# Performance work log

Measured on AMD Instinct MI355X. Metric: run time of the kernel, lower is better.

## Reference

```python
import jax, jax.numpy as jnp
import numpy as np
import math

# Model hyperparameters (SchNet defaults)
H = 128        # hidden_channels
F = 128        # num_filters
G = 50         # num_gaussians
CUT = 6.0      # cutoff (Angstrom)
L_INT = 3      # num_interactions
# Graph scale
N_MOL = 512    # molecules
APM = 32       # atoms per molecule
N = N_MOL * APM
BOX = 10.0     # side of cubic box per molecule


def _ssp(x):
    # ShiftedSoftplus
    return jax.nn.softplus(x) - math.log(2.0)


def setup_inputs() -> dict:
    rng = np.random.default_rng(0)
    pos = rng.uniform(0.0, BOX, (N_MOL, APM, 3)).astype(np.float32)
    # radius graph within each molecule (faithful to radius_graph_custom,
    # precomputed here because edge count is data-dependent)
    srcs, dsts = [], []
    for m in range(N_MOL):
        p = pos[m]
        dm = np.linalg.norm(p[:, None, :] - p[None, :, :], axis=-1)
        mask = dm <= CUT
        np.fill_diagonal(mask, False)
        s, t = np.nonzero(mask)
        srcs.append(s + m * APM)
        dsts.append(t + m * APM)
    edge_index = np.stack([np.concatenate(srcs), np.concatenate(dsts)]).astype(np.int32)
    pos = pos.reshape(N, 3)
    batch = np.repeat(np.arange(N_MOL, dtype=np.int32), APM)
    z = rng.integers(1, 100, N).astype(np.int32)

    key = jax.random.key(0)
    ks = jax.random.split(key, 16)
    s = 0.1
    nrm = lambda k, shp: (jax.random.normal(k, shp, dtype=jnp.float32) * s)
    return {
        "z": jnp.asarray(z),
        "pos": jnp.asarray(pos),
        "batch": jnp.asarray(batch),
        "edge_index": jnp.asarray(edge_index),
        "emb": nrm(ks[0], (100, H)),
        "mlp_w1": nrm(ks[1], (L_INT, G, F)),
        "mlp_b1": jnp.zeros((L_INT, F), jnp.float32),
        "mlp_w2": nrm(ks[2], (L_INT, F, F)),
        "mlp_b2": jnp.zeros((L_INT, F), jnp.float32),
        "cf1_w": nrm(ks[3], (L_INT, H, F)),
        "cf2_w": nrm(ks[4], (L_INT, F, H)),
        "cf2_b": jnp.zeros((L_INT, H), jnp.float32),
        "lin_w": nrm(ks[5], (L_INT, H, H)),
        "lin_b": jnp.zeros((L_INT, H), jnp.float32),
        "out1_w": nrm(ks[6], (H, H // 2)),
        "out1_b": jnp.zeros((H // 2,), jnp.float32),
        "out2_w": nrm(ks[7], (H // 2, 1)),
        "out2_b": jnp.zeros((1,), jnp.float32),
    }


def reference(z, pos, batch, edge_index, emb,
              mlp_w1, mlp_b1, mlp_w2, mlp_b2,
              cf1_w, cf2_w, cf2_b, lin_w, lin_b,
              out1_w, out1_b, out2_w, out2_b):
    src, dst = edge_index[0], edge_index[1]
    # edge_weight = euclidean distance (== cdist[src, dst])
    d = jnp.sqrt(jnp.sum((pos[src] - pos[dst]) ** 2, axis=-1))  # [E]
    # GaussianSmearing
    offs = jnp.linspace(0.0, CUT, G)
    coeff = -0.5 / (CUT / (G - 1)) ** 2
    edge_attr = jnp.exp(coeff * (d[:, None] - offs[None, :]) ** 2)  # [E, G]
    # cosine cutoff
    Ccut = 0.5 * (jnp.cos(d * math.pi / CUT) + 1.0)  # [E]

    h = emb[z]  # [N, H]
    for l in range(L_INT):
        # edge filter MLP with cutoff
        W = _ssp(edge_attr @ mlp_w1[l] + mlp_b1[l]) @ mlp_w2[l] + mlp_b2[l]  # [E, F]
        W = W * Ccut[:, None]
        # CFConv: lin1 -> gather x_j -> multiply -> scatter-add to dst -> lin2
        msg = (h @ cf1_w[l])[src] * W                                # [E, F]
        agg = jax.ops.segment_sum(msg, dst, num_segments=N)          # [N, F]
        v = agg @ cf2_w[l] + cf2_b[l]                                # [N, H]
        v = _ssp(v)
        v = v @ lin_w[l] + lin_b[l]
        h = h + v  # residual

    h = _ssp(h @ out1_w + out1_b)
    h = h @ out2_w + out2_b                                          # [N, 1]
    out = jax.ops.segment_sum(h, batch, num_segments=N_MOL)          # [N_MOL, 1]
    return out
```

## Files before the change

### kernel.cpp

```cpp
#include <hip/hip_runtime.h>
#include <hip/hip_bf16.h>
#include <hip/hip_fp16.h>
#include <math.h>

#define NATOMS 16384
#define NMOL   512
#define APM    32
#define GDIM   50
#define KTAB   4096

#define STRH 132
#define STRA 136

typedef __attribute__((ext_vector_type(8))) short   short8;
typedef __attribute__((ext_vector_type(4))) float   floatx4;

__device__ __forceinline__ float ssp(float x) {
    float e = __expf(-fabsf(x));
    return fmaxf(x, 0.0f) + __logf(1.0f + e) - 0.69314718055994531f;
}

__device__ __forceinline__ unsigned short f2bf(float x) {
    union { float f; unsigned int u; } v; v.f = x;
    unsigned int lsb = (v.u >> 16) & 1u;
    v.u += 0x7fffu + lsb;
    return (unsigned short)(v.u >> 16);
}

__device__ __forceinline__ unsigned short f2h(float x) {
    __half h = __float2half(x);
    unsigned short u;
    __builtin_memcpy(&u, &h, 2);
    return u;
}

__device__ __forceinline__ unsigned int pk2bf(float a, float b) {
    __hip_bfloat162 h = __float22bfloat162_rn(make_float2(a, b));
    unsigned int u;
    __builtin_memcpy(&u, &h, 4);
    return u;
}

#define KW1 72
#define KW2 136
#define NTILE (KTAB / 64)

__global__ __launch_bounds__(256) void mega_setup_kernel(
    const float* __restrict__ pos,
    unsigned* __restrict__ koG,
    const float* __restrict__ cf1, const float* __restrict__ cf2,
    const float* __restrict__ lin, const float* __restrict__ out1,
    unsigned short* __restrict__ Wtall,
    const float* __restrict__ w1_, const float* __restrict__ b1_,
    const float* __restrict__ w2_, const float* __restrict__ b2_,
    unsigned short* __restrict__ Tt)
{
    const int WB = (9 * 16384 + 64 * 128 + 255) / 256;
    const int b = blockIdx.x;
    const int tid = threadIdx.x;

    __shared__ float sp[96];

    if (b < NMOL) {
        if (tid < 96) sp[tid] = pos[b * 96 + tid];
        if (b < 3 && tid < 128)
            Tt[(size_t)b * (KTAB + 1) * 128 + (size_t)KTAB * 128 + tid] = 0;
        __syncthreads();
        #pragma unroll
        for (int c4 = 0; c4 < 4; c4++) {
            int c = c4 * 256 + tid;
            int i = c >> 5, j = c & 31;
            float dx = sp[3 * i]     - sp[3 * j];
            float dy = sp[3 * i + 1] - sp[3 * j + 1];
            float dz = sp[3 * i + 2] - sp[3 * j + 2];
            float d  = sqrtf(dx * dx + dy * dy + dz * dz);
            unsigned off = (unsigned)(KTAB << 8);
            if (i != j && d <= 6.0f) {
                float u = d * (float)(KTAB - 1) / 6.0f;
                int k = min((int)(u + 0.5f), KTAB - 1);
                off = (unsigned)(k << 8);
            }
            koG[((size_t)b << 10) + c] = off;
        }
        return;
    }
    if (b < NMOL + WB) {
        int idx = (b - NMOL) * 256 + tid;
        if (idx < 9 * 16384) {
            int wi = idx >> 14, rem = idx & 16383;
            int n = rem >> 7, k = rem & 127;
            int l = wi / 3, which = wi % 3;
            const float* src = (which == 0) ? cf1 : (which == 1) ? cf2 : lin;
            Wtall[idx] = f2bf(src[(size_t)l * 16384 + k * 128 + n]);
        } else if (idx < 9 * 16384 + 64 * 128) {
            int q = idx - 9 * 16384;
            int n = q >> 7, k = q & 127;
            Wtall[idx] = f2bf(out1[k * 64 + n]);
        }
        return;
    }

    __shared__ unsigned short s_bufA[128 * KW2];
    __shared__ unsigned short s_bufB[128 * KW1];

    const int tt = b - NMOL - WB;
    const int l  = tt / NTILE;
    const int bx = tt % NTILE;
    const float* w1 = w1_ + (size_t)l * GDIM * 128;
    const float* b1 = b1_ + (size_t)l * 128;
    const float* w2 = w2_ + (size_t)l * 128 * 128;
    const float* b2 = b2_ + (size_t)l * 128;
    unsigned short* Tg = Tt + (size_t)l * (KTAB + 1) * 128;

    unsigned short* s_w1T = s_bufB;
    unsigned short* s_w2T = s_bufA;
    unsigned short* s_t   = s_bufB;

    for (int i = tid; i < GDIM * 128; i += 256) {
        int g = i >> 7, f = i & 127;
        s_w1T[f * KW1 + g] = f2bf(w1[i]);
    }
    for (int i = tid; i < (64 - GDIM) * 128; i += 256) {
        int g = GDIM + (i >> 7), f = i & 127;
        s_w1T[f * KW1 + g] = 0;
    }
    for (int i = tid; i < 128 * 128; i += 256) {
        int k = i >> 7, n = i & 127;
        s_w2T[n * KW2 + k] = f2bf(w2[i]);
    }

    const int lane = tid & 63;
    const int w    = tid >> 6;
    const int l15  = lane & 15;
    const int quad = lane >> 4;

    float b1v[8], b2v[8];
    #pragma unroll
    for (int nt = 0; nt < 8; nt++) {
        b1v[nt] = b1[nt * 16 + l15];
        b2v[nt] = b2[nt * 16 + l15];
    }
    __syncthreads();

    const float hstep = 6.0f / (float)(KTAB - 1);
    const float step  = 6.0f / 49.0f;
    const float coeff = -0.5f / (step * step);
    const float pioc  = 3.14159265358979323846f / 6.0f;
    const int k0 = bx * 64;
    const float dm = (float)(k0 + w * 16 + l15) * hstep;

    floatx4 acc1[8];
    #pragma unroll
    for (int nt = 0; nt < 8; nt++) acc1[nt] = (floatx4){0.f, 0.f, 0.f, 0.f};
    #pragma unroll
    for (int ks = 0; ks < 2; ks++) {
        unsigned int ap[4];
        #pragma unroll
        for (int jj = 0; jj < 4; jj++) {
            int g0 = ks * 32 + quad * 8 + 2 * jj;
            float d0 = dm - (float)g0 * step;
            float d1 = dm - (float)(g0 + 1) * step;
            float v0 = (g0 < GDIM)     ? __expf(coeff * d0 * d0) : 0.0f;
            float v1 = (g0 + 1 < GDIM) ? __expf(coeff * d1 * d1) : 0.0f;
            ap[jj] = pk2bf(v0, v1);
        }
        short8 af;
        __builtin_memcpy(&af, ap, 16);
        #pragma unroll
        for (int nt = 0; nt < 8; nt++) {
            short8 bfg = *(const short8*)&s_w1T[(nt * 16 + l15) * KW1 + ks * 32 + quad * 8];
            acc1[nt] = __builtin_amdgcn_mfma_f32_16x16x32_bf16(af, bfg, acc1[nt], 0, 0, 0);
        }
    }
    __syncthreads();

    #pragma unroll
    for (int nt = 0; nt < 8; nt++) {
        #pragma unroll
        for (int r = 0; r < 4; r++) {
            int row = w * 16 + quad * 4 + r;
            s_t[row * KW2 + nt * 16 + l15] = f2bf(ssp(acc1[nt][r] + b1v[nt]));
        }
    }

    floatx4 acc2[8];
    #pragma unroll
    for (int nt = 0; nt < 8; nt++) acc2[nt] = (floatx4){0.f, 0.f, 0.f, 0.f};
    #pragma unroll
    for (int ks = 0; ks < 4; ks++) {
        short8 af = *(const short8*)&s_t[(w * 16 + l15) * KW2 + ks * 32 + quad * 8];
        #pragma unroll
        for (int nt = 0; nt < 8; nt++) {
            short8 bfg = *(const short8*)&s_w2T[(nt * 16 + l15) * KW2 + ks * 32 + quad * 8];
            acc2[nt] = __builtin_amdgcn_mfma_f32_16x16x32_bf16(af, bfg, acc2[nt], 0, 0, 0);
        }
    }

    #pragma unroll
    for (int nt = 0; nt < 8; nt++) {
        #pragma unroll
        for (int r = 0; r < 4; r++) {
            int row = w * 16 + quad * 4 + r;
            float d = (float)(k0 + row) * hstep;
            float cut = 0.5f * (__cosf(d * pioc) + 1.0f);
            Tg[(size_t)(k0 + row) * 128 + nt * 16 + l15] = f2h((acc2[nt][r] + b2v[nt]) * cut);
        }
    }
}

__global__ __launch_bounds__(512, 4) void fused_schnet_kernel(
    const int* __restrict__ z, const float* __restrict__ emb,
    const unsigned* __restrict__ koG,
    const unsigned short* __restrict__ Tt,
    const unsigned short* __restrict__ Wtall,
    const float* __restrict__ cf2_b, const float* __restrict__ lin_b,
    const float* __restrict__ out1_b, const float* __restrict__ out2_w,
    const float* __restrict__ out2_b,
    float* __restrict__ out)
{
    __shared__ float s_h[32 * STRH];
    __shared__ float s_hx[32 * 128];
    __shared__ unsigned short s_agg[32 * STRA];
    __shared__ unsigned int s_ko[32 * 32];
    __shared__ float s_red;
    unsigned short* s_t = (unsigned short*)s_hx;

    const int tid  = threadIdx.x;
    const int lane = tid & 63;
    const int w    = tid >> 6;
    const int l15  = lane & 15;
    const int quad = lane >> 4;
    const int r16  = (w & 1) * 16;
    const int c32  = (w >> 1) * 32;
    const int B0   = blockIdx.x * 32;

    const unsigned lOff = (unsigned)(lane << 2);

    for (int i = tid; i < 32 * 128; i += 512) {
        int row = i >> 7, col = i & 127;
        s_h[row * STRH + col] = emb[(size_t)z[B0 + row] * 128 + col];
    }
    for (int i = tid; i < 1024; i += 512)
        s_ko[i] = koG[((size_t)blockIdx.x << 10) + i];
    if (tid == 0) s_red = 0.0f;

    __syncthreads();

    const unsigned short* WtO = Wtall + 9 * 16384;

#define KO_RFL(KO, SC)                                                        \
    _Pragma("unroll")                                                         \
    for (int i = 0; i < 4; i++) {                                             \
        uint4 ka = *(const uint4*)&s_ko[(((w << 2) + i) << 5) + ((SC) << 3)]; \
        uint4 kb = *(const uint4*)&s_ko[(((w << 2) + i) << 5) + ((SC) << 3) + 4]; \
        KO[i][0] = __builtin_amdgcn_readfirstlane(ka.x);                      \
        KO[i][1] = __builtin_amdgcn_readfirstlane(ka.y);                      \
        KO[i][2] = __builtin_amdgcn_readfirstlane(ka.z);                      \
        KO[i][3] = __builtin_amdgcn_readfirstlane(ka.w);                      \
        KO[i][4] = __builtin_amdgcn_readfirstlane(kb.x);                      \
        KO[i][5] = __builtin_amdgcn_readfirstlane(kb.y);                      \
        KO[i][6] = __builtin_amdgcn_readfirstlane(kb.z);                      \
        KO[i][7] = __builtin_amdgcn_readfirstlane(kb.w);                      \
    }
#define TP_LOAD(TP, KO)                                                       \
    _Pragma("unroll")                                                         \
    for (int i = 0; i < 4; i++) {                                             \
        _Pragma("unroll")                                                     \
        for (int j = 0; j < 8; j++)                                           \
            TP[i][j] = *(const unsigned*)(TlB + KO[i][j] + lOff);             \
    }
#define FMA_CHUNK(TP, SC)                                                     \
    _Pragma("unroll")                                                         \
    for (int j = 0; j < 8; j++) {                                             \
        float2 hv = *(const float2*)&s_hx[((((SC) << 3) + j) << 7) + (lane << 1)]; \
        _Pragma("unroll")                                                     \
        for (int i = 0; i < 4; i++) {                                         \
            unsigned t = TP[i][j];                                            \
            asm("v_fma_mix_f32 %0, %1, %2, %0 op_sel:[0,0,0] op_sel_hi:[1,0,0]" \
                : "+v"(a0[i]) : "v"(t), "v"(hv.x));                           \
            asm("v_fma_mix_f32 %0, %1, %2, %0 op_sel:[1,0,0] op_sel_hi:[1,0,0]" \
                : "+v"(a1[i]) : "v"(t), "v"(hv.y));                           \
        }                                                                     \
    }

    for (int l = 0; l < 3; l++) {
        const unsigned short* W1 = Wtall + (size_t)(l * 3 + 0) * 16384;
        const unsigned short* W2 = Wtall + (size_t)(l * 3 + 1) * 16384;
        const unsigned short* W3 = Wtall + (size_t)(l * 3 + 2) * 16384;
        const char* TlB = (const char*)(Tt + (size_t)l * (KTAB + 1) * 128);

        floatx4 acc[2];
        #pragma unroll
        for (int nt = 0; nt < 2; nt++) acc[nt] = (floatx4){0.f, 0.f, 0.f, 0.f};
        #pragma unroll
        for (int ks = 0; ks < 4; ks++) {
            const float* hp = &s_h[(r16 + l15) * STRH + ks * 32 + quad * 8];
            float4 xa = *(const float4*)hp;
            float4 xb = *(const float4*)(hp + 4);
            unsigned int ap[4];
            ap[0] = pk2bf(xa.x, xa.y); ap[1] = pk2bf(xa.z, xa.w);
            ap[2] = pk2bf(xb.x, xb.y); ap[3] = pk2bf(xb.z, xb.w);
            short8 af;
            __builtin_memcpy(&af, ap, 16);
            #pragma unroll
            for (int nt = 0; nt < 2; nt++) {
                short8 bfg = *(const short8*)&W1[(size_t)(c32 + nt * 16 + l15) * 128 + ks * 32 + quad * 8];
                acc[nt] = __builtin_amdgcn_mfma_f32_16x16x32_bf16(af, bfg, acc[nt], 0, 0, 0);
            }
        }
        #pragma unroll
        for (int nt = 0; nt < 2; nt++) {
            #pragma unroll
            for (int r = 0; r < 4; r++)
                s_hx[(r16 + quad * 4 + r) * 128 + c32 + nt * 16 + l15] = acc[nt][r];
        }

        __syncthreads();

        {
            float a0[4], a1[4];
            #pragma unroll
            for (int i = 0; i < 4; i++) { a0[i] = 0.0f; a1[i] = 0.0f; }

            unsigned koA[4][8], koB[4][8], tpA[4][8], tpB[4][8];
            KO_RFL(koA, 0)
            TP_LOAD(tpA, koA)

            KO_RFL(koB, 1)
            TP_LOAD(tpB, koB)
            FMA_CHUNK(tpA, 0)

            KO_RFL(koA, 2)
            TP_LOAD(tpA, koA)
            FMA_CHUNK(tpB, 1)

            KO_RFL(koB, 3)
            TP_LOAD(tpB, koB)
            FMA_CHUNK(tpA, 2)

            FMA_CHUNK(tpB, 3)

            #pragma unroll
            for (int i = 0; i < 4; i++)
                *(unsigned*)&s_agg[((w << 2) + i) * STRA + (lane << 1)] = pk2bf(a0[i], a1[i]);
        }

        __syncthreads();

        float bva[2], bvb[2];
        #pragma unroll
        for (int nt = 0; nt < 2; nt++) {
            bva[nt] = cf2_b[l * 128 + c32 + nt * 16 + l15];
            bvb[nt] = lin_b[l * 128 + c32 + nt * 16 + l15];
        }
        #pragma unroll
        for (int nt = 0; nt < 2; nt++) acc[nt] = (floatx4){0.f, 0.f, 0.f, 0.f};
        #pragma unroll
        for (int ks = 0; ks < 4; ks++) {
            short8 af = *(const short8*)&s_agg[(r16 + l15) * STRA + ks * 32 + quad * 8];
            #pragma unroll
            for (int nt = 0; nt < 2; nt++) {
                short8 bfg = *(const short8*)&W2[(size_t)(c32 + nt * 16 + l15) * 128 + ks * 32 + quad * 8];
                acc[nt] = __builtin_amdgcn_mfma_f32_16x16x32_bf16(af, bfg, acc[nt], 0, 0, 0);
            }
        }
        #pragma unroll
        for (int nt = 0; nt < 2; nt++) {
            #pragma unroll
            for (int r = 0; r < 4; r++) {
                int row = r16 + quad * 4 + r;
                s_t[row * STRA + c32 + nt * 16 + l15] = f2bf(ssp(acc[nt][r] + bva[nt]));
            }
        }

        __syncthreads();

        #pragma unroll
        for (int nt = 0; nt < 2; nt++) acc[nt] = (floatx4){0.f, 0.f, 0.f, 0.f};
        #pragma unroll
        for (int ks = 0; ks < 4; ks++) {
            short8 af = *(const short8*)&s_t[(r16 + l15) * STRA + ks * 32 + quad * 8];
            #pragma unroll
            for (int nt = 0; nt < 2; nt++) {
                short8 bfg = *(const short8*)&W3[(size_t)(c32 + nt * 16 + l15) * 128 + ks * 32 + quad * 8];
                acc[nt] = __builtin_amdgcn_mfma_f32_16x16x32_bf16(af, bfg, acc[nt], 0, 0, 0);
            }
        }
        #pragma unroll
        for (int nt = 0; nt < 2; nt++) {
            #pragma unroll
            for (int r = 0; r < 4; r++) {
                int row = r16 + quad * 4 + r;
                s_h[row * STRH + c32 + nt * 16 + l15] += acc[nt][r] + bvb[nt];
            }
        }
        __syncthreads();
    }

    const int c16 = (w >> 1) * 16;
    floatx4 ha = (floatx4){0.f, 0.f, 0.f, 0.f};
    #pragma unroll
    for (int ks = 0; ks < 4; ks++) {
        const float* hp = &s_h[(r16 + l15) * STRH + ks * 32 + quad * 8];
        float4 xa = *(const float4*)hp;
        float4 xb = *(const float4*)(hp + 4);
        unsigned int ap[4];
        ap[0] = pk2bf(xa.x, xa.y); ap[1] = pk2bf(xa.z, xa.w);
        ap[2] = pk2bf(xb.x, xb.y); ap[3] = pk2bf(xb.z, xb.w);
        short8 af;
        __builtin_memcpy(&af, ap, 16);
        short8 bfg = *(const short8*)&WtO[(size_t)(c16 + l15) * 128 + ks * 32 + quad * 8];
        ha = __builtin_amdgcn_mfma_f32_16x16x32_bf16(af, bfg, ha, 0, 0, 0);
    }
    float part = 0.0f;
    {
        float b1o = out1_b[c16 + l15];
        float o2  = out2_w[c16 + l15];
        #pragma unroll
        for (int r = 0; r < 4; r++)
            part += ssp(ha[r] + b1o) * o2;
    }
    #pragma unroll
    for (int off = 32; off > 0; off >>= 1) part += __shfl_down(part, off);
    if (lane == 0) atomicAdd(&s_red, part);
    __syncthreads();
    if (tid == 0) out[blockIdx.x] = s_red + 32.0f * out2_b[0];

#undef KO_RFL
#undef TP_LOAD
#undef FMA_CHUNK
}

extern "C" void kernel_launch(void* const* d_in, const int* in_sizes, int n_in,
                              void* d_out, int out_size, void* d_ws, size_t ws_size,
                              hipStream_t stream)
{
    const int*   z      = (const int*)d_in[0];
    const float* pos    = (const float*)d_in[1];
    const float* emb    = (const float*)d_in[4];
    const float* mlp_w1 = (const float*)d_in[5];
    const float* mlp_b1 = (const float*)d_in[6];
    const float* mlp_w2 = (const float*)d_in[7];
    const float* mlp_b2 = (const float*)d_in[8];
    const float* cf1_w  = (const float*)d_in[9];
    const float* cf2_w  = (const float*)d_in[10];
    const float* cf2_b  = (const float*)d_in[11];
    const float* lin_w  = (const float*)d_in[12];
    const float* lin_b  = (const float*)d_in[13];
    const float* out1_w = (const float*)d_in[14];
    const float* out1_b = (const float*)d_in[15];
    const float* out2_w = (const float*)d_in[16];
    const float* out2_b = (const float*)d_in[17];

    char* p = (char*)d_ws;
    unsigned* koG = (unsigned*)p;                 p += (size_t)NMOL * 1024 * 4;
    unsigned short* Tt = (unsigned short*)p;      p += (size_t)3 * (KTAB + 1) * 128 * 2;
    unsigned short* Wtall = (unsigned short*)p;

    const int WB = (9 * 16384 + 64 * 128 + 255) / 256;
    const int TB = NTILE * 3;
    mega_setup_kernel<<<NMOL + WB + TB, 256, 0, stream>>>(
        pos, koG, cf1_w, cf2_w, lin_w, out1_w, Wtall,
        mlp_w1, mlp_b1, mlp_w2, mlp_b2, Tt);

    fused_schnet_kernel<<<NMOL, 512, 0, stream>>>(
        z, emb, koG, Tt, Wtall,
        cf2_b, lin_b, out1_b, out2_w, out2_b, (float*)d_out);
}
```

Baseline: 159.3 us.

## Split setup into weight-conversion and filter-table kernels reading pretransposed global weights

The single setup kernel is split in two. The first converts all weights, including the filter-MLP weights, to transposed bf16 in global memory. The second builds the cutoff-filter lookup table and reads its MFMA B operands straight from those global buffers, no longer staging each layer's weights into shared memory per block. This removes the redundant per-block fp32-to-bf16 transposition of the 128x128 weights in all 192 table blocks, at the cost of an extra kernel launch and a serial dependency between the two setup kernels.

```diff
diff --git a/kernel.cpp b/kernel.cpp
--- a/kernel.cpp
+++ b/kernel.cpp
@@ -41,21 +41,25 @@
     return u;
 }
 
-#define KW1 72
 #define KW2 136
 #define NTILE (KTAB / 64)
 
-__global__ __launch_bounds__(256) void mega_setup_kernel(
+#define N_WTALL  147456
+#define N_OUT1   8192
+#define N_W1T    24576
+#define N_W2T    49152
+#define WB_ELEMS (N_WTALL + N_OUT1 + N_W1T + N_W2T)
+#define WB_BLOCKS (WB_ELEMS / 256)
+
+__global__ __launch_bounds__(256) void setup_a_kernel(
     const float* __restrict__ pos,
     unsigned* __restrict__ koG,
     const float* __restrict__ cf1, const float* __restrict__ cf2,
     const float* __restrict__ lin, const float* __restrict__ out1,
-    unsigned short* __restrict__ Wtall,
-    const float* __restrict__ w1_, const float* __restrict__ b1_,
-    const float* __restrict__ w2_, const float* __restrict__ b2_,
+    const float* __restrict__ w1_, const float* __restrict__ w2_,
+    unsigned short* __restrict__ Wtall, unsigned short* __restrict__ Wmlp,
     unsigned short* __restrict__ Tt)
 {
-    const int WB = (9 * 16384 + 64 * 128 + 255) / 256;
     const int b = blockIdx.x;
     const int tid = threadIdx.x;
 
@@ -84,51 +88,48 @@
         }
         return;
     }
-    if (b < NMOL + WB) {
-        int idx = (b - NMOL) * 256 + tid;
-        if (idx < 9 * 16384) {
-            int wi = idx >> 14, rem = idx & 16383;
-            int n = rem >> 7, k = rem & 127;
-            int l = wi / 3, which = wi % 3;
-            const float* src = (which == 0) ? cf1 : (which == 1) ? cf2 : lin;
-            Wtall[idx] = f2bf(src[(size_t)l * 16384 + k * 128 + n]);
-        } else if (idx < 9 * 16384 + 64 * 128) {
-            int q = idx - 9 * 16384;
-            int n = q >> 7, k = q & 127;
-            Wtall[idx] = f2bf(out1[k * 64 + n]);
-        }
-        return;
-    }
-
-    __shared__ unsigned short s_bufA[128 * KW2];
-    __shared__ unsigned short s_bufB[128 * KW1];
-
-    const int tt = b - NMOL - WB;
+
+    int idx = (b - NMOL) * 256 + tid;
+    if (idx < N_WTALL) {
+        int wi = idx >> 14, rem = idx & 16383;
+        int n = rem >> 7, k = rem & 127;
+        int l = wi / 3, which = wi % 3;
+        const float* src = (which == 0) ? cf1 : (which == 1) ? cf2 : lin;
+        Wtall[idx] = f2bf(src[(size_t)l * 16384 + k * 128 + n]);
+    } else if (idx < N_WTALL + N_OUT1) {
+        int q = idx - N_WTALL;
+        int n = q >> 7, k = q & 127;
+        Wtall[idx] = f2bf(out1[k * 64 + n]);
+    } else if (idx < N_WTALL + N_OUT1 + N_W1T) {
+        int q = idx - (N_WTALL + N_OUT1);
+        int l = q >> 13, rem = q & 8191;
+        int n = rem >> 6, k = rem & 63;
+        Wmlp[q] = (k < GDIM) ? f2bf(w1_[(size_t)l * GDIM * 128 + k * 128 + n]) : 0;
+    } else {
+        int q = idx - (N_WTALL + N_OUT1 + N_W1T);
+        int l = q >> 14, rem = q & 16383;
+        int n = rem >> 7, k = rem & 127;
+        Wmlp[N_W1T + q] = f2bf(w2_[(size_t)l * 16384 + k * 128 + n]);
+    }
+}
+
+__global__ __launch_bounds__(256) void setup_b_kernel(
+    const unsigned short* __restrict__ Wmlp,
+    const float* __restrict__ b1_, const float* __restrict__ b2_,
+    unsigned short* __restrict__ Tt)
+{
+    __shared__ unsigned short s_t[64 * KW2];
+
+    const int tt = blockIdx.x;
     const int l  = tt / NTILE;
     const int bx = tt % NTILE;
-    const float* w1 = w1_ + (size_t)l * GDIM * 128;
+    const unsigned short* W1g = Wmlp + (size_t)l * 8192;
+    const unsigned short* W2g = Wmlp + N_W1T + (size_t)l * 16384;
     const float* b1 = b1_ + (size_t)l * 128;
-    const float* w2 = w2_ + (size_t)l * 128 * 128;
     const float* b2 = b2_ + (size_t)l * 128;
     unsigned short* Tg = Tt + (size_t)l * (KTAB + 1) * 128;
 
-    unsigned short* s_w1T = s_bufB;
-    unsigned short* s_w2T = s_bufA;
-    unsigned short* s_t   = s_bufB;
-
-    for (int i = tid; i < GDIM * 128; i += 256) {
-        int g = i >> 7, f = i & 127;
-        s_w1T[f * KW1 + g] = f2bf(w1[i]);
-    }
-    for (int i = tid; i < (64 - GDIM) * 128; i += 256) {
-        int g = GDIM + (i >> 7), f = i & 127;
-        s_w1T[f * KW1 + g] = 0;
-    }
-    for (int i = tid; i < 128 * 128; i += 256) {
-        int k = i >> 7, n = i & 127;
-        s_w2T[n * KW2 + k] = f2bf(w2[i]);
-    }
-
+    const int tid  = threadIdx.x;
     const int lane = tid & 63;
     const int w    = tid >> 6;
     const int l15  = lane & 15;
@@ -140,7 +141,6 @@
         b1v[nt] = b1[nt * 16 + l15];
         b2v[nt] = b2[nt * 16 + l15];
     }
-    __syncthreads();
 
     const float hstep = 6.0f / (float)(KTAB - 1);
     const float step  = 6.0f / 49.0f;
@@ -168,11 +168,10 @@
         __builtin_memcpy(&af, ap, 16);
         #pragma unroll
         for (int nt = 0; nt < 8; nt++) {
-            short8 bfg = *(const short8*)&s_w1T[(nt * 16 + l15) * KW1 + ks * 32 + quad * 8];
+            short8 bfg = *(const short8*)&W1g[(nt * 16 + l15) * 64 + ks * 32 + quad * 8];
             acc1[nt] = __builtin_amdgcn_mfma_f32_16x16x32_bf16(af, bfg, acc1[nt], 0, 0, 0);
         }
     }
-    __syncthreads();
 
     #pragma unroll
     for (int nt = 0; nt < 8; nt++) {
@@ -191,7 +190,7 @@
         short8 af = *(const short8*)&s_t[(w * 16 + l15) * KW2 + ks * 32 + quad * 8];
         #pragma unroll
         for (int nt = 0; nt < 8; nt++) {
-            short8 bfg = *(const short8*)&s_w2T[(nt * 16 + l15) * KW2 + ks * 32 + quad * 8];
+            short8 bfg = *(const short8*)&W2g[(nt * 16 + l15) * 128 + ks * 32 + quad * 8];
             acc2[nt] = __builtin_amdgcn_mfma_f32_16x16x32_bf16(af, bfg, acc2[nt], 0, 0, 0);
         }
     }
@@ -455,13 +454,15 @@
     char* p = (char*)d_ws;
     unsigned* koG = (unsigned*)p;                 p += (size_t)NMOL * 1024 * 4;
     unsigned short* Tt = (unsigned short*)p;      p += (size_t)3 * (KTAB + 1) * 128 * 2;
-    unsigned short* Wtall = (unsigned short*)p;
-
-    const int WB = (9 * 16384 + 64 * 128 + 255) / 256;
-    const int TB = NTILE * 3;
-    mega_setup_kernel<<<NMOL + WB + TB, 256, 0, stream>>>(
-        pos, koG, cf1_w, cf2_w, lin_w, out1_w, Wtall,
-        mlp_w1, mlp_b1, mlp_w2, mlp_b2, Tt);
+    unsigned short* Wtall = (unsigned short*)p;   p += ((size_t)(N_WTALL + N_OUT1) * 2 + 63) & ~63ULL;
+    unsigned short* Wmlp = (unsigned short*)p;
+
+    setup_a_kernel<<<NMOL + WB_BLOCKS, 256, 0, stream>>>(
+        pos, koG, cf1_w, cf2_w, lin_w, out1_w, mlp_w1, mlp_w2,
+        Wtall, Wmlp, Tt);
+
+    setup_b_kernel<<<NTILE * 3, 256, 0, stream>>>(
+        Wmlp, mlp_b1, mlp_b2, Tt);
 
     fused_schnet_kernel<<<NMOL, 512, 0, stream>>>(
         z, emb, koG, Tt, Wtall,
```

Measured after the change: 157.9 us, median of 2. No clear change (-0.9%).
